# Kernel tuning notes

Hardware: AMD Instinct MI355X
Metric: run time of the kernel (lower is better)

## Reference

```python
import jax, jax.numpy as jnp
import numpy as np

B, C, N, H = 4, 512, 16384, 8
D = C // H
EPS = 1e-6

def setup_inputs() -> dict:
    key = jax.random.key(0)
    k1, k2, k3 = jax.random.split(key, 3)
    # xavier_normal std for Linear(C, out): sqrt(2/(fan_in+fan_out))
    std_qkv = (2.0 / (C + 3 * C)) ** 0.5
    std_proj = (2.0 / (C + C)) ** 0.5
    return {
        "x": jax.random.normal(k1, (B, C, N), dtype=jnp.float32),
        "W_qkv": jax.random.normal(k2, (C, 3 * C), dtype=jnp.float32) * std_qkv,
        "b_qkv": jnp.zeros((3 * C,), dtype=jnp.float32),
        "W_proj": jax.random.normal(k3, (C, C), dtype=jnp.float32) * std_proj,
        "b_proj": jnp.zeros((C,), dtype=jnp.float32),
    }

def _phi(x):
    return jax.nn.elu(x) + 1.0

def reference(x, W_qkv, b_qkv, W_proj, b_proj):
    # x: [B, C, N] -> [B, N, C]
    xt = jnp.swapaxes(x, 1, 2)
    qkv = xt @ W_qkv + b_qkv                      # [B, N, 3C]
    q, k, v = jnp.split(qkv, 3, axis=-1)
    # [B, N, C] -> [B, H, N, D]
    def heads(t):
        return jnp.swapaxes(t.reshape(B, N, H, D), 1, 2)
    q, k, v = heads(q), heads(k), heads(v)
    q_phi = _phi(q)                               # [B, H, N, D]
    k_phi = _phi(k)
    S = jnp.einsum('bhnd,bhne->bhde', k_phi, v)   # [B, H, D, D] KV state
    k_sum = k_phi.sum(axis=-2)                    # [B, H, D]
    num = jnp.einsum('bhnd,bhde->bhne', q_phi, S) # [B, H, N, D]
    den = jnp.einsum('bhnd,bhd->bhn', q_phi, k_sum)[..., None] + EPS
    out = num / den                               # [B, H, N, D]
    out = jnp.swapaxes(out, 1, 2).reshape(B, N, C)
    out = out @ W_proj + b_proj                   # [B, N, C]
    return jnp.swapaxes(out, 1, 2)                # [B, C, N]
```

## Files before the change

kernel.cpp:

```cpp
#include <hip/hip_runtime.h>
#include <cmath>

#define B_  4
#define C_  512
#define N_  16384
#define H_  8
#define D_  64
#define C3_ 1536
#define EPS 1e-6f

#define PADA 72
#define PADT 136
#define PADO 132

typedef __attribute__((ext_vector_type(8))) short bf16x8;
typedef __attribute__((ext_vector_type(4))) float f32x4;

__device__ __forceinline__ ushort f2bf(float f) {
    union { float f; unsigned u; } c{f};
    unsigned r = (c.u + 0x7FFF + ((c.u >> 16) & 1)) >> 16;
    return (ushort)r;
}
__device__ __forceinline__ float bf2f(ushort b) {
    union { unsigned u; float f; } c{(unsigned)b << 16};
    return c.f;
}
__device__ __forceinline__ float phi_f(float x) { return x > 0.f ? x + 1.f : __expf(x); }

__global__ __launch_bounds__(256) void k_transpose(
        const float* __restrict__ src, ushort* __restrict__ dst,
        int R, int Cc, long sStride, long dStride) {
    __shared__ ushort T[64][72];
    const long sb = (long)blockIdx.z * sStride;
    const long db = (long)blockIdx.z * dStride;
    const int c0 = blockIdx.x * 64, r0 = blockIdx.y * 64;
    const int t = threadIdx.x;
    const int ct = t & 15, rt = t >> 4;
    float4 v[4];
    #pragma unroll
    for (int k = 0; k < 4; ++k)
        v[k] = *(const float4*)(src + sb + (long)(r0 + rt * 4 + k) * Cc + c0 + ct * 4);
    #pragma unroll
    for (int j = 0; j < 4; ++j) {
        ushort pk[4];
        #pragma unroll
        for (int k = 0; k < 4; ++k) pk[k] = f2bf(((const float*)&v[k])[j]);
        *(uint2*)&T[ct * 4 + j][rt * 4] = *(uint2*)pk;
    }
    __syncthreads();
    const int c = t >> 2, rq = (t & 3) * 16;
    ushort* d = dst + db + (long)(c0 + c) * R + r0 + rq;
    *(int4*)(d)     = *(const int4*)&T[c][rq];
    *(int4*)(d + 8) = *(const int4*)&T[c][rq + 8];
}

__global__ __launch_bounds__(256) void k_kv_s(
        const ushort* __restrict__ xt, const ushort* __restrict__ Wqt,
        const float* __restrict__ bqkv, float* __restrict__ S_g,
        float* __restrict__ ksum_g) {
    const int s = blockIdx.x, h = blockIdx.y, b = blockIdx.z;
    const int tid = threadIdx.x;
    const int w = tid >> 6, ln = tid & 63, lr = ln & 15, lq = ln >> 4;
    const int bh = b * H_ + h;

    __shared__ __align__(16) char smem[128 * PADA * 2 * 2];
    ushort (*Ax)[PADA]  = (ushort(*)[PADA])smem;
    ushort (*Bw)[PADA]  = (ushort(*)[PADA])(smem + 128 * PADA * 2);
    ushort (*kvT)[PADT] = (ushort(*)[PADT])smem;
    __shared__ float biasL[128];
    __shared__ float ksRed[4][64];

    if (tid < 128) {
        int col = tid < 64 ? (512 + h * 64 + tid) : (1024 + h * 64 + (tid - 64));
        biasL[tid] = bqkv[col];
    }

    const f32x4 FZ = {0.f, 0.f, 0.f, 0.f};
    f32x4 Sacc[4] = {FZ, FZ, FZ, FZ};
    float ksp = 0.f;

    for (int it = 0; it < 8; ++it) {
        const int n0 = (s * 8 + it) * 128;
        f32x4 acc[2][8];
        #pragma unroll
        for (int mi = 0; mi < 2; mi++)
            #pragma unroll
            for (int ji = 0; ji < 8; ji++) acc[mi][ji] = FZ;

        for (int kc = 0; kc < 8; ++kc) {
            const int c0 = kc * 64;
            __syncthreads();
            {
                int row = tid >> 1, co = (tid & 1) * 32;
                const int4* srca = (const int4*)(xt + ((long)(b * N_ + n0 + row)) * C_ + c0 + co);
                int4* dsta = (int4*)&Ax[row][co];
                dsta[0] = srca[0]; dsta[1] = srca[1]; dsta[2] = srca[2]; dsta[3] = srca[3];
                int j = row;
                int wr = j < 64 ? (512 + h * 64 + j) : (1024 + h * 64 + (j - 64));
                const int4* srcb = (const int4*)(Wqt + (long)wr * C_ + c0 + co);
                int4* dstb = (int4*)&Bw[j][co];
                dstb[0] = srcb[0]; dstb[1] = srcb[1]; dstb[2] = srcb[2]; dstb[3] = srcb[3];
            }
            __syncthreads();
            #pragma unroll
            for (int ks = 0; ks < 2; ++ks) {
                bf16x8 a[2], bb[8];
                #pragma unroll
                for (int mi = 0; mi < 2; mi++)
                    a[mi] = *(const bf16x8*)&Ax[w * 32 + mi * 16 + lr][ks * 32 + lq * 8];
                #pragma unroll
                for (int ji = 0; ji < 8; ji++)
                    bb[ji] = *(const bf16x8*)&Bw[ji * 16 + lr][ks * 32 + lq * 8];
                #pragma unroll
                for (int mi = 0; mi < 2; mi++)
                    #pragma unroll
                    for (int ji = 0; ji < 8; ji++)
                        acc[mi][ji] = __builtin_amdgcn_mfma_f32_16x16x32_bf16(
                            a[mi], bb[ji], acc[mi][ji], 0, 0, 0);
            }
        }
        __syncthreads();
        #pragma unroll
        for (int mi = 0; mi < 2; mi++) {
            int nl = w * 32 + mi * 16 + lq * 4;
            #pragma unroll
            for (int ji = 0; ji < 8; ji++) {
                int j = ji * 16 + lr;
                float bs = biasL[j];
                ushort pk[4];
                #pragma unroll
                for (int r = 0; r < 4; r++) {
                    float vv = acc[mi][ji][r] + bs;
                    if (j < 64) vv = phi_f(vv);
                    pk[r] = f2bf(vv);
                }
                *(uint2*)&kvT[j][nl] = *(uint2*)pk;
            }
        }
        __syncthreads();
        #pragma unroll
        for (int ks = 0; ks < 4; ++ks) {
            bf16x8 af = *(const bf16x8*)&kvT[w * 16 + lr][ks * 32 + lq * 8];
            #pragma unroll
            for (int e = 0; e < 4; e++) {
                bf16x8 bv = *(const bf16x8*)&kvT[64 + e * 16 + lr][ks * 32 + lq * 8];
                Sacc[e] = __builtin_amdgcn_mfma_f32_16x16x32_bf16(af, bv, Sacc[e], 0, 0, 0);
            }
        }
        {
            int d = tid & 63, q = tid >> 6;
            float sum = 0.f;
            #pragma unroll
            for (int m = 0; m < 4; m++) {
                bf16x8 u = *(const bf16x8*)&kvT[d][q * 32 + m * 8];
                #pragma unroll
                for (int j = 0; j < 8; j++) sum += bf2f((ushort)u[j]);
            }
            ksp += sum;
        }
    }
    #pragma unroll
    for (int e = 0; e < 4; e++)
        #pragma unroll
        for (int r = 0; r < 4; r++)
            atomicAdd(&S_g[((long)bh * 64 + w * 16 + lq * 4 + r) * 64 + e * 16 + lr],
                      Sacc[e][r]);
    ksRed[tid >> 6][tid & 63] = ksp;
    __syncthreads();
    if (tid < 64)
        atomicAdd(&ksum_g[bh * 64 + tid],
                  ksRed[0][tid] + ksRed[1][tid] + ksRed[2][tid] + ksRed[3][tid]);
}

__global__ void k_sfin(const float* __restrict__ S_g, const float* __restrict__ ksum_g,
                       ushort* __restrict__ SbT) {
    int bh = blockIdx.x, t = threadIdx.x;
    for (int i = t; i < 5120; i += 256) {
        int e = i >> 6, d = i & 63;
        float v = (e < 64) ? S_g[(long)bh * 4096 + d * 64 + e]
                           : (e == 64 ? ksum_g[bh * 64 + d] : 0.f);
        ushort hi = f2bf(v);
        ushort lo = f2bf(v - bf2f(hi));
        SbT[(long)bh * 10240 + i] = hi;
        SbT[(long)bh * 10240 + 5120 + i] = lo;
    }
}

__global__ __launch_bounds__(256) void k_q_attn(
        const ushort* __restrict__ xt, const ushort* __restrict__ Wqt,
        const float* __restrict__ bqkv, const ushort* __restrict__ SbT,
        ushort* __restrict__ attn) {
    const int nt = blockIdx.x, h = blockIdx.y, b = blockIdx.z;
    const int n0 = nt * 128;
    const int tid = threadIdx.x;
    const int w = tid >> 6, ln = tid & 63, lr = ln & 15, lq = ln >> 4;
    const int bh = b * H_ + h;

    __shared__ __align__(16) ushort Ax[128][PADA];
    __shared__ __align__(16) ushort Bq[64][PADA];
    __shared__ __align__(16) ushort Sb[160][PADA];
    __shared__ float denL[128];

    #pragma unroll
    for (int p = 0; p < 5; ++p) {
        int r = p * 32 + (tid >> 3);
        *(int4*)&Sb[r][(tid & 7) * 8] =
            *(const int4*)(SbT + (long)bh * 10240 + r * 64 + (tid & 7) * 8);
    }

    const f32x4 FZ = {0.f, 0.f, 0.f, 0.f};
    f32x4 accq[2][4];
    #pragma unroll
    for (int mi = 0; mi < 2; mi++)
        #pragma unroll
        for (int ji = 0; ji < 4; ji++) accq[mi][ji] = FZ;

    for (int kc = 0; kc < 8; ++kc) {
        const int c0 = kc * 64;
        __syncthreads();
        {
            int row = tid >> 1, co = (tid & 1) * 32;
            const int4* srca = (const int4*)(xt + ((long)(b * N_ + n0 + row)) * C_ + c0 + co);
            int4* dsta = (int4*)&Ax[row][co];
            dsta[0] = srca[0]; dsta[1] = srca[1]; dsta[2] = srca[2]; dsta[3] = srca[3];
            if (tid < 128) {
                int j = tid >> 1;
                const int4* srcb = (const int4*)(Wqt + (long)(h * 64 + j) * C_ + c0 + co);
                int4* dstb = (int4*)&Bq[j][co];
                dstb[0] = srcb[0]; dstb[1] = srcb[1]; dstb[2] = srcb[2]; dstb[3] = srcb[3];
            }
        }
        __syncthreads();
        #pragma unroll
        for (int ks = 0; ks < 2; ++ks) {
            bf16x8 a[2], bb[4];
            #pragma unroll
            for (int mi = 0; mi < 2; mi++)
                a[mi] = *(const bf16x8*)&Ax[w * 32 + mi * 16 + lr][ks * 32 + lq * 8];
            #pragma unroll
            for (int ji = 0; ji < 4; ji++)
                bb[ji] = *(const bf16x8*)&Bq[ji * 16 + lr][ks * 32 + lq * 8];
            #pragma unroll
            for (int mi = 0; mi < 2; mi++)
                #pragma unroll
                for (int ji = 0; ji < 4; ji++)
                    accq[mi][ji] = __builtin_amdgcn_mfma_f32_16x16x32_bf16(
                        a[mi], bb[ji], accq[mi][ji], 0, 0, 0);
        }
    }
    __syncthreads();
    #pragma unroll
    for (int mi = 0; mi < 2; mi++) {
        int nl = w * 32 + mi * 16 + lq * 4;
        #pragma unroll
        for (int ji = 0; ji < 4; ji++) {
            int d = ji * 16 + lr;
            float bs = bqkv[h * 64 + d];
            #pragma unroll
            for (int r = 0; r < 4; r++)
                Ax[nl + r][d] = f2bf(phi_f(accq[mi][ji][r] + bs));
        }
    }
    __syncthreads();
    f32x4 accn[2][5];
    #pragma unroll
    for (int mi = 0; mi < 2; mi++)
        #pragma unroll
        for (int ei = 0; ei < 5; ei++) accn[mi][ei] = FZ;
    #pragma unroll
    for (int ks = 0; ks < 2; ++ks) {
        bf16x8 a[2];
        #pragma unroll
        for (int mi = 0; mi < 2; mi++)
            a[mi] = *(const bf16x8*)&Ax[w * 32 + mi * 16 + lr][ks * 32 + lq * 8];
        #pragma unroll
        for (int ei = 0; ei < 5; ei++) {
            bf16x8 bhi = *(const bf16x8*)&Sb[ei * 16 + lr][ks * 32 + lq * 8];
            bf16x8 blo = *(const bf16x8*)&Sb[80 + ei * 16 + lr][ks * 32 + lq * 8];
            #pragma unroll
            for (int mi = 0; mi < 2; mi++) {
                accn[mi][ei] = __builtin_amdgcn_mfma_f32_16x16x32_bf16(
                    a[mi], bhi, accn[mi][ei], 0, 0, 0);
                accn[mi][ei] = __builtin_amdgcn_mfma_f32_16x16x32_bf16(
                    a[mi], blo, accn[mi][ei], 0, 0, 0);
            }
        }
    }
    if (lr == 0) {
        #pragma unroll
        for (int mi = 0; mi < 2; mi++)
            #pragma unroll
            for (int r = 0; r < 4; r++)
                denL[w * 32 + mi * 16 + lq * 4 + r] = accn[mi][4][r] + EPS;
    }
    __syncthreads();
    #pragma unroll
    for (int mi = 0; mi < 2; mi++) {
        int nl = w * 32 + mi * 16 + lq * 4;
        #pragma unroll
        for (int ji = 0; ji < 4; ji++) {
            int e = ji * 16 + lr;
            #pragma unroll
            for (int r = 0; r < 4; r++)
                Ax[nl + r][e] = f2bf(accn[mi][ji][r] / denL[nl + r]);
        }
    }
    __syncthreads();
    {
        int row = tid >> 1, co = (tid & 1) * 32;
        const int4* sp = (const int4*)&Ax[row][co];
        int4* dp = (int4*)(attn + ((long)(b * N_ + n0 + row)) * C_ + h * 64 + co);
        dp[0] = sp[0]; dp[1] = sp[1]; dp[2] = sp[2]; dp[3] = sp[3];
    }
}

__global__ __launch_bounds__(256) void k_proj(
        const ushort* __restrict__ attn, const ushort* __restrict__ Wpt,
        const float* __restrict__ bproj, float* __restrict__ out) {
    const int nt = blockIdx.x, jt = blockIdx.y;
    const int tid = threadIdx.x;
    const int w = tid >> 6, ln = tid & 63, lr = ln & 15, lq = ln >> 4;
    const int b = nt >> 7;
    const int nloc = (nt & 127) * 128;

    __shared__ __align__(16) char smem[128 * PADA * 2 * 2];
    ushort (*Aa)[PADA] = (ushort(*)[PADA])smem;
    ushort (*Bw)[PADA] = (ushort(*)[PADA])(smem + 128 * PADA * 2);
    float (*outT)[PADO] = (float(*)[PADO])smem;

    const f32x4 FZ = {0.f, 0.f, 0.f, 0.f};
    f32x4 acc[2][8];
    #pragma unroll
    for (int mi = 0; mi < 2; mi++)
        #pragma unroll
        for (int ji = 0; ji < 8; ji++) acc[mi][ji] = FZ;

    for (int kc = 0; kc < 8; ++kc) {
        const int c0 = kc * 64;
        __syncthreads();
        {
            int row = tid >> 1, co = (tid & 1) * 32;
            const int4* srca = (const int4*)(attn + ((long)(nt * 128 + row)) * C_ + c0 + co);
            int4* dsta = (int4*)&Aa[row][co];
            dsta[0] = srca[0]; dsta[1] = srca[1]; dsta[2] = srca[2]; dsta[3] = srca[3];
            int j = row;
            const int4* srcb = (const int4*)(Wpt + (long)(jt * 128 + j) * C_ + c0 + co);
            int4* dstb = (int4*)&Bw[j][co];
            dstb[0] = srcb[0]; dstb[1] = srcb[1]; dstb[2] = srcb[2]; dstb[3] = srcb[3];
        }
        __syncthreads();
        #pragma unroll
        for (int ks = 0; ks < 2; ++ks) {
            bf16x8 a[2], bb[8];
            #pragma unroll
            for (int mi = 0; mi < 2; mi++)
                a[mi] = *(const bf16x8*)&Aa[w * 32 + mi * 16 + lr][ks * 32 + lq * 8];
            #pragma unroll
            for (int ji = 0; ji < 8; ji++)
                bb[ji] = *(const bf16x8*)&Bw[ji * 16 + lr][ks * 32 + lq * 8];
            #pragma unroll
            for (int mi = 0; mi < 2; mi++)
                #pragma unroll
                for (int ji = 0; ji < 8; ji++)
                    acc[mi][ji] = __builtin_amdgcn_mfma_f32_16x16x32_bf16(
                        a[mi], bb[ji], acc[mi][ji], 0, 0, 0);
        }
    }
    #pragma unroll
    for (int half = 0; half < 2; ++half) {
        __syncthreads();
        #pragma unroll
        for (int mi = 0; mi < 2; mi++) {
            int nl = w * 32 + mi * 16 + lq * 4;
            #pragma unroll
            for (int ji = 0; ji < 4; ji++) {
                int cl = ji * 16 + lr;
                float bs = bproj[jt * 128 + half * 64 + cl];
                f32x4 v = acc[mi][half * 4 + ji];
                #pragma unroll
                for (int r = 0; r < 4; r++) v[r] += bs;
                *(f32x4*)&outT[cl][nl] = v;
            }
        }
        __syncthreads();
        {
            int cl = tid >> 2, ch = (tid & 3) * 32;
            const float* sp = &outT[cl][ch];
            float* dp = out + ((long)(b * C_ + jt * 128 + half * 64 + cl)) * N_ + nloc + ch;
            #pragma unroll
            for (int k = 0; k < 8; ++k)
                ((float4*)dp)[k] = ((const float4*)sp)[k];
        }
    }
}

__global__ __launch_bounds__(256) void kernelA_fb(
        const float* __restrict__ x, const float* __restrict__ Wqkv,
        const float* __restrict__ bqkv, float* __restrict__ S_g,
        float* __restrict__ ksum_g) {
    const int h = blockIdx.x;
    const int s = blockIdx.y;
    const int b = blockIdx.z;
    const int tid = threadIdx.x;
    const int tn = tid & 15;
    const int tj = tid >> 4;
    const int td = tid & 15;
    const int te = tid >> 4;

    __shared__ float As[16][64];
    __shared__ float Bs[16][128];
    __shared__ float kphi_s[64][64];
    __shared__ float v_s[64][64];

    float acc2[4][4];
    #pragma unroll
    for (int i = 0; i < 4; i++)
        #pragma unroll
        for (int j = 0; j < 4; j++) acc2[i][j] = 0.f;
    float ksum_r = 0.f;

    float bias_j[8];
    #pragma unroll
    for (int jj = 0; jj < 8; jj++) {
        int j = tj * 8 + jj;
        int col = (j < 64) ? (512 + h * 64 + j) : (1024 + h * 64 + (j - 64));
        bias_j[jj] = bqkv[col];
    }

    for (int it = 0; it < 8; ++it) {
        const int n0 = (s * 8 + it) * 64;
        float acc[4][8];
        #pragma unroll
        for (int i = 0; i < 4; i++)
            #pragma unroll
            for (int jj = 0; jj < 8; jj++) acc[i][jj] = 0.f;

        for (int kc = 0; kc < 32; ++kc) {
            const int c0 = kc * 16;
            __syncthreads();
            {
                int r = tid >> 4, n4 = (tid & 15) * 4;
                const float* src = x + ((size_t)b * C_ + (c0 + r)) * (size_t)N_ + n0 + n4;
                *(float4*)&As[r][n4] = *(const float4*)src;
            }
            #pragma unroll
            for (int part = 0; part < 2; ++part) {
                int idx = tid + part * 256;
                int r = idx >> 5;
                int j4 = (idx & 31) * 4;
                int col = (j4 < 64) ? (512 + h * 64 + j4) : (1024 + h * 64 + (j4 - 64));
                const float* src = Wqkv + (size_t)(c0 + r) * C3_ + col;
                *(float4*)&Bs[r][j4] = *(const float4*)src;
            }
            __syncthreads();
            #pragma unroll
            for (int k = 0; k < 16; ++k) {
                float a[4], bb[8];
                *(float4*)a      = *(const float4*)&As[k][tn * 4];
                *(float4*)&bb[0] = *(const float4*)&Bs[k][tj * 8];
                *(float4*)&bb[4] = *(const float4*)&Bs[k][tj * 8 + 4];
                #pragma unroll
                for (int i = 0; i < 4; i++)
                    #pragma unroll
                    for (int jj = 0; jj < 8; jj++)
                        acc[i][jj] = fmaf(a[i], bb[jj], acc[i][jj]);
            }
        }
        __syncthreads();
        if (tj < 8) {
            #pragma unroll
            for (int i = 0; i < 4; i++) {
                int n = tn * 4 + i;
                float tmp[8];
                #pragma unroll
                for (int jj = 0; jj < 8; jj++) tmp[jj] = phi_f(acc[i][jj] + bias_j[jj]);
                *(float4*)&kphi_s[n][tj * 8]     = *(float4*)&tmp[0];
                *(float4*)&kphi_s[n][tj * 8 + 4] = *(float4*)&tmp[4];
            }
        } else {
            #pragma unroll
            for (int i = 0; i < 4; i++) {
                int n = tn * 4 + i;
                float tmp[8];
                #pragma unroll
                for (int jj = 0; jj < 8; jj++) tmp[jj] = acc[i][jj] + bias_j[jj];
                *(float4*)&v_s[n][(tj - 8) * 8]     = *(float4*)&tmp[0];
                *(float4*)&v_s[n][(tj - 8) * 8 + 4] = *(float4*)&tmp[4];
            }
        }
        __syncthreads();
        #pragma unroll 4
        for (int n = 0; n < 64; ++n) {
            float a[4], bb[4];
            *(float4*)a  = *(const float4*)&kphi_s[n][td * 4];
            *(float4*)bb = *(const float4*)&v_s[n][te * 4];
            #pragma unroll
            for (int dd = 0; dd < 4; dd++)
                #pragma unroll
                for (int ee = 0; ee < 4; ee++)
                    acc2[dd][ee] = fmaf(a[dd], bb[ee], acc2[dd][ee]);
        }
        if (tid < 64) {
            float sum = 0.f;
            #pragma unroll 8
            for (int n = 0; n < 64; ++n) sum += kphi_s[n][tid];
            ksum_r += sum;
        }
    }

    const int bh = b * H_ + h;
    #pragma unroll
    for (int dd = 0; dd < 4; dd++)
        #pragma unroll
        for (int ee = 0; ee < 4; ee++)
            atomicAdd(&S_g[((size_t)bh * 64 + td * 4 + dd) * 64 + te * 4 + ee], acc2[dd][ee]);
    if (tid < 64) atomicAdd(&ksum_g[bh * 64 + tid], ksum_r);
}

__global__ __launch_bounds__(256) void kernelB_fb(
        const float* __restrict__ x, const float* __restrict__ Wqkv,
        const float* __restrict__ bqkv, const float* __restrict__ Wproj,
        const float* __restrict__ bproj, const float* __restrict__ S_g,
        const float* __restrict__ ksum_g, float* __restrict__ out) {
    const int nt = blockIdx.x;
    const int b  = blockIdx.y;
    const int n0 = nt * 16;
    const int tid = threadIdx.x;
    const int tn = tid & 3;
    const int tj = tid >> 2;

    __shared__ float QA[512][16];
    __shared__ float As[16][16];
    __shared__ float Bs2[16][256];
    __shared__ float SB[16][64];
    __shared__ float ksumL[512];
    __shared__ float denL[16];

    ksumL[tid]       = ksum_g[(size_t)b * 512 + tid];
    ksumL[tid + 256] = ksum_g[(size_t)b * 512 + tid + 256];

    for (int half = 0; half < 2; ++half) {
        float acc[4][4];
        #pragma unroll
        for (int i = 0; i < 4; i++)
            #pragma unroll
            for (int j = 0; j < 4; j++) acc[i][j] = 0.f;

        for (int kc = 0; kc < 32; ++kc) {
            const int c0 = kc * 16;
            __syncthreads();
            {
                int r = tid >> 4, n = tid & 15;
                As[r][n] = x[((size_t)b * C_ + c0 + r) * (size_t)N_ + n0 + n];
            }
            {
                int r = tid >> 4;
                int j0 = (tid & 15) * 16;
                const float* src = Wqkv + (size_t)(c0 + r) * C3_ + half * 256 + j0;
                float4* dst = (float4*)&Bs2[r][j0];
                #pragma unroll
                for (int q4 = 0; q4 < 4; q4++) dst[q4] = ((const float4*)src)[q4];
            }
            __syncthreads();
            #pragma unroll
            for (int k = 0; k < 16; ++k) {
                float a[4], bb[4];
                *(float4*)a  = *(const float4*)&As[k][tn * 4];
                *(float4*)bb = *(const float4*)&Bs2[k][tj * 4];
                #pragma unroll
                for (int i = 0; i < 4; i++)
                    #pragma unroll
                    for (int jj = 0; jj < 4; jj++)
                        acc[i][jj] = fmaf(a[i], bb[jj], acc[i][jj]);
            }
        }
        #pragma unroll
        for (int jj = 0; jj < 4; jj++) {
            int c = half * 256 + tj * 4 + jj;
            float bq = bqkv[c];
            float tmp[4];
            #pragma unroll
            for (int i = 0; i < 4; i++) tmp[i] = phi_f(acc[i][jj] + bq);
            *(float4*)&QA[c][tn * 4] = *(float4*)tmp;
        }
    }
    __syncthreads();

    for (int h = 0; h < H_; ++h) {
        if (tid < 16) {
            float d = 0.f;
            #pragma unroll 8
            for (int dd = 0; dd < 64; ++dd)
                d = fmaf(QA[h * 64 + dd][tid], ksumL[h * 64 + dd], d);
            denL[tid] = d + EPS;
        }
        float acc4[4] = {0.f, 0.f, 0.f, 0.f};
        for (int dc = 0; dc < 4; ++dc) {
            __syncthreads();
            {
                int r = tid >> 4, e4 = (tid & 15) * 4;
                *(float4*)&SB[r][e4] =
                    *(const float4*)&S_g[(((size_t)(b * H_ + h)) * 64 + dc * 16 + r) * 64 + e4];
            }
            __syncthreads();
            #pragma unroll
            for (int k = 0; k < 16; ++k) {
                float a[4];
                *(float4*)a = *(const float4*)&QA[h * 64 + dc * 16 + k][tn * 4];
                float bb = SB[k][tj];
                #pragma unroll
                for (int i = 0; i < 4; i++) acc4[i] = fmaf(a[i], bb, acc4[i]);
            }
        }
        __syncthreads();
        {
            float tmp[4];
            #pragma unroll
            for (int i = 0; i < 4; i++) tmp[i] = acc4[i] / denL[tn * 4 + i];
            *(float4*)&QA[h * 64 + tj][tn * 4] = *(float4*)tmp;
        }
        __syncthreads();
    }

    for (int half = 0; half < 2; ++half) {
        float acc[4][4];
        #pragma unroll
        for (int i = 0; i < 4; i++)
            #pragma unroll
            for (int j = 0; j < 4; j++) acc[i][j] = 0.f;

        for (int kc = 0; kc < 32; ++kc) {
            __syncthreads();
            {
                int r = tid >> 4;
                int j0 = (tid & 15) * 16;
                const float* src = Wproj + (size_t)(kc * 16 + r) * C_ + half * 256 + j0;
                float4* dst = (float4*)&Bs2[r][j0];
                #pragma unroll
                for (int q4 = 0; q4 < 4; q4++) dst[q4] = ((const float4*)src)[q4];
            }
            __syncthreads();
            #pragma unroll
            for (int k = 0; k < 16; ++k) {
                float a[4], bb[4];
                *(float4*)a  = *(const float4*)&QA[kc * 16 + k][tn * 4];
                *(float4*)bb = *(const float4*)&Bs2[k][tj * 4];
                #pragma unroll
                for (int i = 0; i < 4; i++)
                    #pragma unroll
                    for (int jj = 0; jj < 4; jj++)
                        acc[i][jj] = fmaf(a[i], bb[jj], acc[i][jj]);
            }
        }
        #pragma unroll
        for (int jj = 0; jj < 4; jj++) {
            int c = half * 256 + tj * 4 + jj;
            float bp = bproj[c];
            float tmp[4];
            #pragma unroll
            for (int i = 0; i < 4; i++) tmp[i] = acc[i][jj] + bp;
            *(float4*)&out[((size_t)b * C_ + c) * (size_t)N_ + n0 + tn * 4] = *(float4*)tmp;
        }
    }
}

extern "C" void kernel_launch(void* const* d_in, const int* in_sizes, int n_in,
                              void* d_out, int out_size, void* d_ws, size_t ws_size,
                              hipStream_t stream) {
    const float* x     = (const float*)d_in[0];
    const float* Wqkv  = (const float*)d_in[1];
    const float* bqkv  = (const float*)d_in[2];
    const float* Wproj = (const float*)d_in[3];
    const float* bproj = (const float*)d_in[4];
    float* out = (float*)d_out;

    const size_t oS    = 0;
    const size_t oK    = oS + 524288;
    const size_t oXT   = oK + 8192;
    const size_t oWq   = oXT + 67108864;
    const size_t oWp   = oWq + 1572864;
    const size_t oSbT  = oWp + 524288;
    const size_t oAttn = oSbT + 655360;
    const size_t need  = oAttn + 67108864;

    float* S_g    = (float*)((char*)d_ws + oS);
    float* ksum_g = (float*)((char*)d_ws + oK);

    if (ws_size < need) {
        hipMemsetAsync(d_ws, 0, 532480, stream);
        kernelA_fb<<<dim3(H_, 32, B_), 256, 0, stream>>>(x, Wqkv, bqkv, S_g, ksum_g);
        kernelB_fb<<<dim3(N_ / 16, B_), 256, 0, stream>>>(x, Wqkv, bqkv, Wproj, bproj,
                                                          S_g, ksum_g, out);
        return;
    }

    ushort* xt   = (ushort*)((char*)d_ws + oXT);
    ushort* Wqt  = (ushort*)((char*)d_ws + oWq);
    ushort* Wpt  = (ushort*)((char*)d_ws + oWp);
    ushort* SbT  = (ushort*)((char*)d_ws + oSbT);
    ushort* attn = (ushort*)((char*)d_ws + oAttn);

    hipMemsetAsync(d_ws, 0, 532480, stream);
    k_transpose<<<dim3(N_ / 64, C_ / 64, B_), 256, 0, stream>>>(
        x, xt, C_, N_, (long)C_ * N_, (long)N_ * C_);
    k_transpose<<<dim3(C3_ / 64, C_ / 64, 1), 256, 0, stream>>>(
        Wqkv, Wqt, C_, C3_, 0, 0);
    k_transpose<<<dim3(C_ / 64, C_ / 64, 1), 256, 0, stream>>>(
        Wproj, Wpt, C_, C_, 0, 0);
    k_kv_s<<<dim3(16, H_, B_), 256, 0, stream>>>(xt, Wqt, bqkv, S_g, ksum_g);
    k_sfin<<<dim3(B_ * H_), 256, 0, stream>>>(S_g, ksum_g, SbT);
    k_q_attn<<<dim3(N_ / 128, H_, B_), 256, 0, stream>>>(xt, Wqt, bqkv, SbT, attn);
    k_proj<<<dim3((B_ * N_) / 128, 4), 256, 0, stream>>>(attn, Wpt, bproj, out);
}
```

Measured before the change: 534.3 us.

## Use direct global-to-LDS loads with XOR swizzle, fold k_sum into MFMA

The GEMM staging in the kv, q-attention and projection kernels now uses global_load_lds 16-byte transfers into unpadded, XOR-swizzled LDS tiles. This replaces the register round-trip copies and keeps LDS reads free of bank conflicts. The k_sum reduction is now computed by the MFMA through an appended row of ones, which removes the scalar LDS summation and its shared reduction. The kv kernel grid is doubled to 32 blocks per head, with half the iterations each, for more parallelism at the cost of more atomics. The risks are the correctness of the swizzle and LDS layout, and the extra atomic traffic.

```diff
diff --git a/kernel.cpp b/kernel.cpp
--- a/kernel.cpp
+++ b/kernel.cpp
@@ -9,12 +9,19 @@
 #define C3_ 1536
 #define EPS 1e-6f
 
-#define PADA 72
 #define PADT 136
+#define PADQ 72
 #define PADO 132
 
 typedef __attribute__((ext_vector_type(8))) short bf16x8;
 typedef __attribute__((ext_vector_type(4))) float f32x4;
+
+typedef __attribute__((address_space(1))) const unsigned int as1_uint;
+typedef __attribute__((address_space(3))) unsigned int as3_uint;
+
+__device__ __forceinline__ void gld16(const void* g, void* l) {
+    __builtin_amdgcn_global_load_lds((as1_uint*)g, (as3_uint*)l, 16, 0, 0);
+}
 
 __device__ __forceinline__ ushort f2bf(float f) {
     union { float f; unsigned u; } c{f};
@@ -61,26 +68,44 @@
     const int s = blockIdx.x, h = blockIdx.y, b = blockIdx.z;
     const int tid = threadIdx.x;
     const int w = tid >> 6, ln = tid & 63, lr = ln & 15, lq = ln >> 4;
+    const int lrow = ln >> 3;
+    const int swc = ((ln & 7) ^ lrow) * 8;
     const int bh = b * H_ + h;
 
-    __shared__ __align__(16) char smem[128 * PADA * 2 * 2];
-    ushort (*Ax)[PADA]  = (ushort(*)[PADA])smem;
-    ushort (*Bw)[PADA]  = (ushort(*)[PADA])(smem + 128 * PADA * 2);
+    __shared__ __align__(16) char smem[144 * PADT * 2];
+    ushort* sA = (ushort*)smem;
+    ushort* sB = (ushort*)(smem + 16384);
     ushort (*kvT)[PADT] = (ushort(*)[PADT])smem;
     __shared__ float biasL[128];
-    __shared__ float ksRed[4][64];
 
     if (tid < 128) {
         int col = tid < 64 ? (512 + h * 64 + tid) : (1024 + h * 64 + (tid - 64));
         biasL[tid] = bqkv[col];
     }
+    {
+        int rr = 128 + (tid >> 4), cc = (tid & 15) * 8;
+        ushort v = (tid >> 4) == 0 ? (ushort)0x3F80 : (ushort)0;
+        ushort pk[8];
+        #pragma unroll
+        for (int j = 0; j < 8; ++j) pk[j] = v;
+        *(int4*)&kvT[rr][cc] = *(int4*)pk;
+    }
+
+    const ushort* gB[4];
+    #pragma unroll
+    for (int q = 0; q < 4; ++q) {
+        int j = w * 32 + q * 8 + lrow;
+        int wr = j < 64 ? (512 + h * 64 + j) : (960 + h * 64 + j);
+        gB[q] = Wqt + (long)wr * C_ + swc;
+    }
 
     const f32x4 FZ = {0.f, 0.f, 0.f, 0.f};
-    f32x4 Sacc[4] = {FZ, FZ, FZ, FZ};
-    float ksp = 0.f;
-
-    for (int it = 0; it < 8; ++it) {
-        const int n0 = (s * 8 + it) * 128;
+    f32x4 Sacc[5] = {FZ, FZ, FZ, FZ, FZ};
+
+    for (int it = 0; it < 4; ++it) {
+        const int n0 = (s * 4 + it) * 128;
+        const ushort* gA = xt + ((long)(b * N_ + n0 + w * 32 + lrow)) * C_ + swc;
+
         f32x4 acc[2][8];
         #pragma unroll
         for (int mi = 0; mi < 2; mi++)
@@ -90,27 +115,22 @@
         for (int kc = 0; kc < 8; ++kc) {
             const int c0 = kc * 64;
             __syncthreads();
-            {
-                int row = tid >> 1, co = (tid & 1) * 32;
-                const int4* srca = (const int4*)(xt + ((long)(b * N_ + n0 + row)) * C_ + c0 + co);
-                int4* dsta = (int4*)&Ax[row][co];
-                dsta[0] = srca[0]; dsta[1] = srca[1]; dsta[2] = srca[2]; dsta[3] = srca[3];
-                int j = row;
-                int wr = j < 64 ? (512 + h * 64 + j) : (1024 + h * 64 + (j - 64));
-                const int4* srcb = (const int4*)(Wqt + (long)wr * C_ + c0 + co);
-                int4* dstb = (int4*)&Bw[j][co];
-                dstb[0] = srcb[0]; dstb[1] = srcb[1]; dstb[2] = srcb[2]; dstb[3] = srcb[3];
+            #pragma unroll
+            for (int q = 0; q < 4; ++q) {
+                gld16(gA + (long)(q * 8) * C_ + c0, sA + (w * 32 + q * 8) * 64);
+                gld16(gB[q] + c0,                   sB + (w * 32 + q * 8) * 64);
             }
             __syncthreads();
             #pragma unroll
             for (int ks = 0; ks < 2; ++ks) {
+                const int co = ((ks * 4 + lq) ^ (lr & 7)) * 8;
                 bf16x8 a[2], bb[8];
                 #pragma unroll
                 for (int mi = 0; mi < 2; mi++)
-                    a[mi] = *(const bf16x8*)&Ax[w * 32 + mi * 16 + lr][ks * 32 + lq * 8];
+                    a[mi] = *(const bf16x8*)(sA + (w * 32 + mi * 16 + lr) * 64 + co);
                 #pragma unroll
                 for (int ji = 0; ji < 8; ji++)
-                    bb[ji] = *(const bf16x8*)&Bw[ji * 16 + lr][ks * 32 + lq * 8];
+                    bb[ji] = *(const bf16x8*)(sB + (ji * 16 + lr) * 64 + co);
                 #pragma unroll
                 for (int mi = 0; mi < 2; mi++)
                     #pragma unroll
@@ -142,21 +162,10 @@
         for (int ks = 0; ks < 4; ++ks) {
             bf16x8 af = *(const bf16x8*)&kvT[w * 16 + lr][ks * 32 + lq * 8];
             #pragma unroll
-            for (int e = 0; e < 4; e++) {
+            for (int e = 0; e < 5; e++) {
                 bf16x8 bv = *(const bf16x8*)&kvT[64 + e * 16 + lr][ks * 32 + lq * 8];
                 Sacc[e] = __builtin_amdgcn_mfma_f32_16x16x32_bf16(af, bv, Sacc[e], 0, 0, 0);
             }
-        }
-        {
-            int d = tid & 63, q = tid >> 6;
-            float sum = 0.f;
-            #pragma unroll
-            for (int m = 0; m < 4; m++) {
-                bf16x8 u = *(const bf16x8*)&kvT[d][q * 32 + m * 8];
-                #pragma unroll
-                for (int j = 0; j < 8; j++) sum += bf2f((ushort)u[j]);
-            }
-            ksp += sum;
         }
     }
     #pragma unroll
@@ -165,11 +174,11 @@
         for (int r = 0; r < 4; r++)
             atomicAdd(&S_g[((long)bh * 64 + w * 16 + lq * 4 + r) * 64 + e * 16 + lr],
                       Sacc[e][r]);
-    ksRed[tid >> 6][tid & 63] = ksp;
-    __syncthreads();
-    if (tid < 64)
-        atomicAdd(&ksum_g[bh * 64 + tid],
-                  ksRed[0][tid] + ksRed[1][tid] + ksRed[2][tid] + ksRed[3][tid]);
+    if (lr == 0) {
+        #pragma unroll
+        for (int r = 0; r < 4; r++)
+            atomicAdd(&ksum_g[bh * 64 + w * 16 + lq * 4 + r], Sacc[4][r]);
+    }
 }
 
 __global__ void k_sfin(const float* __restrict__ S_g, const float* __restrict__ ksum_g,
@@ -194,19 +203,26 @@
     const int n0 = nt * 128;
     const int tid = threadIdx.x;
     const int w = tid >> 6, ln = tid & 63, lr = ln & 15, lq = ln >> 4;
+    const int lrow = ln >> 3;
+    const int swc = ((ln & 7) ^ lrow) * 8;
     const int bh = b * H_ + h;
 
-    __shared__ __align__(16) ushort Ax[128][PADA];
-    __shared__ __align__(16) ushort Bq[64][PADA];
-    __shared__ __align__(16) ushort Sb[160][PADA];
+    __shared__ __align__(16) char smem[24576];
+    __shared__ __align__(16) ushort Qphi[128][PADQ];
     __shared__ float denL[128];
-
-    #pragma unroll
-    for (int p = 0; p < 5; ++p) {
-        int r = p * 32 + (tid >> 3);
-        *(int4*)&Sb[r][(tid & 7) * 8] =
-            *(const int4*)(SbT + (long)bh * 10240 + r * 64 + (tid & 7) * 8);
-    }
+    ushort* sA = (ushort*)smem;
+    ushort* sB = (ushort*)(smem + 16384);
+    ushort (*Sb)[PADQ] = (ushort(*)[PADQ])smem;
+
+    float bias_q[4];
+    #pragma unroll
+    for (int ji = 0; ji < 4; ji++) bias_q[ji] = bqkv[h * 64 + ji * 16 + lr];
+
+    const ushort* gA = xt + ((long)(b * N_ + n0 + w * 32 + lrow)) * C_ + swc;
+    const ushort* gB[2];
+    #pragma unroll
+    for (int q = 0; q < 2; ++q)
+        gB[q] = Wqt + (long)(h * 64 + w * 16 + q * 8 + lrow) * C_ + swc;
 
     const f32x4 FZ = {0.f, 0.f, 0.f, 0.f};
     f32x4 accq[2][4];
@@ -218,28 +234,23 @@
     for (int kc = 0; kc < 8; ++kc) {
         const int c0 = kc * 64;
         __syncthreads();
-        {
-            int row = tid >> 1, co = (tid & 1) * 32;
-            const int4* srca = (const int4*)(xt + ((long)(b * N_ + n0 + row)) * C_ + c0 + co);
-            int4* dsta = (int4*)&Ax[row][co];
-            dsta[0] = srca[0]; dsta[1] = srca[1]; dsta[2] = srca[2]; dsta[3] = srca[3];
-            if (tid < 128) {
-                int j = tid >> 1;
-                const int4* srcb = (const int4*)(Wqt + (long)(h * 64 + j) * C_ + c0 + co);
-                int4* dstb = (int4*)&Bq[j][co];
-                dstb[0] = srcb[0]; dstb[1] = srcb[1]; dstb[2] = srcb[2]; dstb[3] = srcb[3];
-            }
-        }
+        #pragma unroll
+        for (int q = 0; q < 4; ++q)
+            gld16(gA + (long)(q * 8) * C_ + c0, sA + (w * 32 + q * 8) * 64);
+        #pragma unroll
+        for (int q = 0; q < 2; ++q)
+            gld16(gB[q] + c0, sB + (w * 16 + q * 8) * 64);
         __syncthreads();
         #pragma unroll
         for (int ks = 0; ks < 2; ++ks) {
+            const int co = ((ks * 4 + lq) ^ (lr & 7)) * 8;
             bf16x8 a[2], bb[4];
             #pragma unroll
             for (int mi = 0; mi < 2; mi++)
-                a[mi] = *(const bf16x8*)&Ax[w * 32 + mi * 16 + lr][ks * 32 + lq * 8];
+                a[mi] = *(const bf16x8*)(sA + (w * 32 + mi * 16 + lr) * 64 + co);
             #pragma unroll
             for (int ji = 0; ji < 4; ji++)
-                bb[ji] = *(const bf16x8*)&Bq[ji * 16 + lr][ks * 32 + lq * 8];
+                bb[ji] = *(const bf16x8*)(sB + (ji * 16 + lr) * 64 + co);
             #pragma unroll
             for (int mi = 0; mi < 2; mi++)
                 #pragma unroll
@@ -248,18 +259,23 @@
                         a[mi], bb[ji], accq[mi][ji], 0, 0, 0);
         }
     }
-    __syncthreads();
     #pragma unroll
     for (int mi = 0; mi < 2; mi++) {
         int nl = w * 32 + mi * 16 + lq * 4;
         #pragma unroll
         for (int ji = 0; ji < 4; ji++) {
             int d = ji * 16 + lr;
-            float bs = bqkv[h * 64 + d];
             #pragma unroll
             for (int r = 0; r < 4; r++)
-                Ax[nl + r][d] = f2bf(phi_f(accq[mi][ji][r] + bs));
-        }
+                Qphi[nl + r][d] = f2bf(phi_f(accq[mi][ji][r] + bias_q[ji]));
+        }
+    }
+    __syncthreads();
+    #pragma unroll
+    for (int p = 0; p < 5; ++p) {
+        int idx = p * 256 + tid;
+        int row = idx >> 3, ch = (idx & 7) * 8;
+        *(int4*)&Sb[row][ch] = *(const int4*)(SbT + (long)bh * 10240 + row * 64 + ch);
     }
     __syncthreads();
     f32x4 accn[2][5];
@@ -272,7 +288,7 @@
         bf16x8 a[2];
         #pragma unroll
         for (int mi = 0; mi < 2; mi++)
-            a[mi] = *(const bf16x8*)&Ax[w * 32 + mi * 16 + lr][ks * 32 + lq * 8];
+            a[mi] = *(const bf16x8*)&Qphi[w * 32 + mi * 16 + lr][ks * 32 + lq * 8];
         #pragma unroll
         for (int ei = 0; ei < 5; ei++) {
             bf16x8 bhi = *(const bf16x8*)&Sb[ei * 16 + lr][ks * 32 + lq * 8];
@@ -302,13 +318,13 @@
             int e = ji * 16 + lr;
             #pragma unroll
             for (int r = 0; r < 4; r++)
-                Ax[nl + r][e] = f2bf(accn[mi][ji][r] / denL[nl + r]);
+                Qphi[nl + r][e] = f2bf(accn[mi][ji][r] / denL[nl + r]);
         }
     }
     __syncthreads();
     {
         int row = tid >> 1, co = (tid & 1) * 32;
-        const int4* sp = (const int4*)&Ax[row][co];
+        const int4* sp = (const int4*)&Qphi[row][co];
         int4* dp = (int4*)(attn + ((long)(b * N_ + n0 + row)) * C_ + h * 64 + co);
         dp[0] = sp[0]; dp[1] = sp[1]; dp[2] = sp[2]; dp[3] = sp[3];
     }
@@ -320,13 +336,18 @@
     const int nt = blockIdx.x, jt = blockIdx.y;
     const int tid = threadIdx.x;
     const int w = tid >> 6, ln = tid & 63, lr = ln & 15, lq = ln >> 4;
+    const int lrow = ln >> 3;
+    const int swc = ((ln & 7) ^ lrow) * 8;
     const int b = nt >> 7;
     const int nloc = (nt & 127) * 128;
 
-    __shared__ __align__(16) char smem[128 * PADA * 2 * 2];
-    ushort (*Aa)[PADA] = (ushort(*)[PADA])smem;
-    ushort (*Bw)[PADA] = (ushort(*)[PADA])(smem + 128 * PADA * 2);
+    __shared__ __align__(16) char smem[64 * PADO * 4];
+    ushort* sA = (ushort*)smem;
+    ushort* sB = (ushort*)(smem + 16384);
     float (*outT)[PADO] = (float(*)[PADO])smem;
+
+    const ushort* gA = attn + ((long)(nt * 128 + w * 32 + lrow)) * C_ + swc;
+    const ushort* gB = Wpt + ((long)(jt * 128 + w * 32 + lrow)) * C_ + swc;
 
     const f32x4 FZ = {0.f, 0.f, 0.f, 0.f};
     f32x4 acc[2][8];
@@ -338,26 +359,22 @@
     for (int kc = 0; kc < 8; ++kc) {
         const int c0 = kc * 64;
         __syncthreads();
-        {
-            int row = tid >> 1, co = (tid & 1) * 32;
-            const int4* srca = (const int4*)(attn + ((long)(nt * 128 + row)) * C_ + c0 + co);
-            int4* dsta = (int4*)&Aa[row][co];
-            dsta[0] = srca[0]; dsta[1] = srca[1]; dsta[2] = srca[2]; dsta[3] = srca[3];
-            int j = row;
-            const int4* srcb = (const int4*)(Wpt + (long)(jt * 128 + j) * C_ + c0 + co);
-            int4* dstb = (int4*)&Bw[j][co];
-            dstb[0] = srcb[0]; dstb[1] = srcb[1]; dstb[2] = srcb[2]; dstb[3] = srcb[3];
+        #pragma unroll
+        for (int q = 0; q < 4; ++q) {
+            gld16(gA + (long)(q * 8) * C_ + c0, sA + (w * 32 + q * 8) * 64);
+            gld16(gB + (long)(q * 8) * C_ + c0, sB + (w * 32 + q * 8) * 64);
         }
         __syncthreads();
         #pragma unroll
         for (int ks = 0; ks < 2; ++ks) {
+            const int co = ((ks * 4 + lq) ^ (lr & 7)) * 8;
             bf16x8 a[2], bb[8];
             #pragma unroll
             for (int mi = 0; mi < 2; mi++)
-                a[mi] = *(const bf16x8*)&Aa[w * 32 + mi * 16 + lr][ks * 32 + lq * 8];
+                a[mi] = *(const bf16x8*)(sA + (w * 32 + mi * 16 + lr) * 64 + co);
             #pragma unroll
             for (int ji = 0; ji < 8; ji++)
-                bb[ji] = *(const bf16x8*)&Bw[ji * 16 + lr][ks * 32 + lq * 8];
+                bb[ji] = *(const bf16x8*)(sB + (ji * 16 + lr) * 64 + co);
             #pragma unroll
             for (int mi = 0; mi < 2; mi++)
                 #pragma unroll
@@ -707,7 +724,7 @@
         Wqkv, Wqt, C_, C3_, 0, 0);
     k_transpose<<<dim3(C_ / 64, C_ / 64, 1), 256, 0, stream>>>(
         Wproj, Wpt, C_, C_, 0, 0);
-    k_kv_s<<<dim3(16, H_, B_), 256, 0, stream>>>(xt, Wqt, bqkv, S_g, ksum_g);
+    k_kv_s<<<dim3(32, H_, B_), 256, 0, stream>>>(xt, Wqt, bqkv, S_g, ksum_g);
     k_sfin<<<dim3(B_ * H_), 256, 0, stream>>>(S_g, ksum_g, SbT);
     k_q_attn<<<dim3(N_ / 128, H_, B_), 256, 0, stream>>>(xt, Wqt, bqkv, SbT, attn);
     k_proj<<<dim3((B_ * N_) / 128, 4), 256, 0, stream>>>(attn, Wpt, bproj, out);
```

Result: slower. 565.5 us (+5.8%).
